# Optimization experiments

Hardware: AMD Instinct MI355X
Metric: run time of the kernel (lower is better)

Reference implementation:

```python
import jax, jax.numpy as jnp
import numpy as np

N_NODES, N_EDGES, NNZ = 10000, 4000, 30000
IN_CH, HEADS, OUT_CH = 128, 2, 64


def _scale2_pattern(node, edge, num_nodes, num_edges):
    """Sparsity pattern of H @ (H^T H) where H is the node x edge incidence.
    Mirrors torch.sparse.mm + coalesce + (values > 0) mask (pattern only,
    since all values are positive sums of ones)."""
    # unique incidence pattern (coalesce)
    uk = np.unique(node.astype(np.int64) * num_edges + edge.astype(np.int64))
    n_u, e_u = uk // num_edges, uk % num_edges
    # --- stage 1: pattern of H^T H = edge pairs sharing a node ---
    order = np.argsort(n_u, kind="stable")
    ns, es = n_u[order], e_u[order]
    _, starts, cnts = np.unique(ns, return_index=True, return_counts=True)
    cpe = np.repeat(cnts, cnts)          # group size per sorted entry
    gpe = np.repeat(starts, cnts)        # group start per sorted entry
    tot = int(cpe.sum())
    within = np.arange(tot) - np.repeat(np.cumsum(cpe) - cpe, cpe)
    pe = np.repeat(es, cpe)
    pep = es[np.repeat(gpe, cpe) + within]
    pk = np.unique(pe * num_edges + pep)
    pe, pep = pk // num_edges, pk % num_edges
    # --- stage 2: pattern of H @ (H^T H) ---
    po = np.argsort(pe, kind="stable")
    pe_s, pep_s = pe[po], pep[po]
    cnt_e = np.bincount(pe_s, minlength=num_edges)
    ptr = np.concatenate([np.zeros(1, np.int64), np.cumsum(cnt_e)])
    c2 = cnt_e[e_u]
    tot2 = int(c2.sum())
    within2 = np.arange(tot2) - np.repeat(np.cumsum(c2) - c2, c2)
    v2 = np.repeat(n_u, c2)
    ep2 = pep_s[ptr[e_u].repeat(c2) + within2]
    k2 = np.unique(v2 * num_edges + ep2)
    return k2 // num_edges, k2 % num_edges


def setup_inputs() -> dict:
    rng = np.random.default_rng(0)
    node1 = rng.integers(0, N_NODES, NNZ).astype(np.int64)
    edge1 = rng.integers(0, N_EDGES, NNZ).astype(np.int64)
    node2, edge2 = _scale2_pattern(node1, edge1, N_NODES, N_EDGES)

    key = jax.random.key(0)
    k = jax.random.split(key, 4)
    HO = HEADS * OUT_CH
    xav1 = (2.0 / (IN_CH + HO)) ** 0.5
    xavo = (2.0 / (HO + OUT_CH)) ** 0.5
    return {
        "x": jax.random.normal(k[0], (N_NODES, IN_CH), jnp.float32),
        "hyperedge_index1": jnp.asarray(np.stack([node1, edge1]), jnp.int32),
        "hyperedge_index2": jnp.asarray(np.stack([node2, edge2]), jnp.int32),
        "W1": jax.random.normal(k[1], (HO, IN_CH), jnp.float32) * xav1,
        "b1": jnp.zeros((HO,), jnp.float32),
        "W2": jax.random.normal(k[2], (HO, IN_CH), jnp.float32) * xav1,
        "b2": jnp.zeros((HO,), jnp.float32),
        "Wout": jax.random.normal(k[3], (OUT_CH, HO), jnp.float32) * xavo,
        "bout": jnp.zeros((OUT_CH,), jnp.float32),
        "num_edges": N_EDGES,
    }


def _hconv(x, W, b, node_idx, edge_idx, num_edges):
    num_nodes = x.shape[0]
    xt = x @ W.T + b                                  # [N, H*O]
    g = xt[node_idx]                                  # [nnz, H*O] gather
    esum = jax.ops.segment_sum(g, edge_idx, num_segments=num_edges)
    cnt = jax.ops.segment_sum(jnp.ones(edge_idx.shape, xt.dtype), edge_idx,
                              num_segments=num_edges)
    emean = esum / jnp.maximum(cnt, 1.0)[:, None]     # scatter_mean (0 if empty)
    return jax.ops.segment_sum(emean[edge_idx], node_idx,
                               num_segments=num_nodes)  # scatter_add


def reference(x, hyperedge_index1, hyperedge_index2, W1, b1, W2, b2, Wout, bout,
              num_edges):
    o1 = _hconv(x, W1, b1, hyperedge_index1[0], hyperedge_index1[1], num_edges)
    o2 = _hconv(x, W2, b2, hyperedge_index2[0], hyperedge_index2[1], num_edges)
    o = 0.5 * (o1 + o2)                               # mean over 2 scales
    return o @ Wout.T + bout                          # output_proj
```

## Files before the change

kernel.cpp:

```cpp
#include <hip/hip_runtime.h>
#include <hip/hip_bf16.h>

#define N_NODES 10000
#define N_EDGES 4000
#define IN_CH   128
#define CHUNK   16384

#define G_GEMM  625
#define G_NPTR  40

__device__ __forceinline__ float bf2f(unsigned short u) {
    union { unsigned int i; float f; } v;
    v.i = ((unsigned int)u) << 16;
    return v.f;
}
__device__ __forceinline__ unsigned short f2bfu(float f) {
    union { __hip_bfloat16 h; unsigned short u; } v;
    v.h = __float2bfloat16(f);
    return v.u;
}

__device__ __forceinline__ void load8(const void* base, size_t eoff, int isf32,
                                      float o[8]) {
    if (isf32) {
        const float4* q = (const float4*)((const float*)base + eoff);
        float4 a = q[0], b = q[1];
        o[0]=a.x; o[1]=a.y; o[2]=a.z; o[3]=a.w;
        o[4]=b.x; o[5]=b.y; o[6]=b.z; o[7]=b.w;
    } else {
        uint4 v = *(const uint4*)((const unsigned short*)base + eoff);
        const unsigned short* pv = (const unsigned short*)&v;
#pragma unroll
        for (int q = 0; q < 8; q++) o[q] = bf2f(pv[q]);
    }
}

__device__ __forceinline__ float loadS(const void* base, int i, int isf32) {
    return isf32 ? ((const float*)base)[i] : bf2f(((const unsigned short*)base)[i]);
}

__device__ __forceinline__ int probe_isf32(const unsigned int* __restrict__ x) {
    const int lane = threadIdx.x & 63;
    unsigned int w0 = x[lane * 2], w1 = x[lane * 2 + 1];
    int h = 0, z = 0;
    {
        unsigned int lo = w0 & 0xFFFFu;
        if (lo == 0u) z++; else if (((lo >> 7) & 0xFF) >= 0x90u) h++;
        lo = w1 & 0xFFFFu;
        if (lo == 0u) z++; else if (((lo >> 7) & 0xFF) >= 0x90u) h++;
    }
    unsigned long long bh = __ballot(h > 0);
    unsigned long long bz = __ballot(z == 2);
    return (__popcll(bh) > 8 || __popcll(bz) > 50) ? 1 : 0;
}

__device__ __forceinline__ void add4(float acc[4], uint2 u) {
    acc[0] += bf2f((unsigned short)(u.x & 0xFFFFu));
    acc[1] += bf2f((unsigned short)(u.x >> 16));
    acc[2] += bf2f((unsigned short)(u.y & 0xFFFFu));
    acc[3] += bf2f((unsigned short)(u.y >> 16));
}

__device__ __forceinline__ void block_scan(const int* __restrict__ cnt, int nb,
                                           int* __restrict__ out,
                                           int* __restrict__ part)
{
    const int t = threadIdx.x;
    const int K = (nb + 255) >> 8;
    const int base = t * K;
    int s = 0;
    for (int q = 0; q < K; q++) { int i = base + q; s += (i < nb) ? cnt[i] : 0; }
    part[t] = s;
    __syncthreads();
    for (int d = 1; d < 256; d <<= 1) {
        int v = (t >= d) ? part[t - d] : 0;
        __syncthreads();
        part[t] += v;
        __syncthreads();
    }
    int run = part[t] - s;
    for (int q = 0; q < K; q++) {
        int i = base + q;
        if (i < nb) { out[i] = run; run += cnt[i]; }
    }
    if (t == 255) out[nb] = part[255];
    __syncthreads();
}

__global__ __launch_bounds__(256) void weff_zero(
    const void* __restrict__ Wout,
    const void* __restrict__ W1, const void* __restrict__ b1,
    const void* __restrict__ W2, const void* __restrict__ b2,
    float* __restrict__ weff1, float* __restrict__ beff1,
    float* __restrict__ weff2, float* __restrict__ beff2,
    int* __restrict__ cntz, int* __restrict__ fillz,
    const unsigned int* __restrict__ xprobe)
{
    const int b = blockIdx.x;
    if (b == 4) {
        for (int t = threadIdx.x; t < 18000; t += 256) cntz[t] = 0;
        for (int t = threadIdx.x; t < 14000; t += 256) fillz[t] = 0;
        return;
    }
    __shared__ float wsh[64][IN_CH];
    const int isf32 = probe_isf32(xprobe);

    if (b == 5) {
        float* bsh = &wsh[0][0];
        const int t = threadIdx.x;
        {
            const int s = t >> 7, h = t & 127;
            bsh[t] = loadS(s ? b2 : b1, h, isf32);
        }
        __syncthreads();
        if (t < 128) {
            const int s = t >> 6, o = t & 63;
            float a = 0.f;
#pragma unroll 4
            for (int r = 0; r < 16; r++) {
                float v[8];
                load8(Wout, (size_t)o * 128 + r * 8, isf32, v);
#pragma unroll
                for (int q = 0; q < 8; q++) a += v[q] * bsh[s * 128 + r * 8 + q];
            }
            (s ? beff2 : beff1)[o] = 0.5f * a;
        }
        return;
    }

    const int s  = b >> 1;
    const int oh = b & 1;
    const void* Ws = s ? W2 : W1;
    float* outW = s ? weff2 : weff1;
    const int o  = oh * 32 + (threadIdx.x >> 3);
    const int i0 = (threadIdx.x & 7) * 16;
    float acc[16];
#pragma unroll
    for (int k = 0; k < 16; k++) acc[k] = 0.f;

    for (int pass = 0; pass < 2; pass++) {
        if (pass) __syncthreads();
        for (int r = 0; r < 4; r++) {
            int idx = r * 2048 + threadIdx.x * 8;
            float v[8];
            load8(Ws, (size_t)pass * 8192 + idx, isf32, v);
            float* d = &wsh[0][0] + idx;
#pragma unroll
            for (int q = 0; q < 8; q++) d[q] = v[q];
        }
        float wrow[64];
#pragma unroll
        for (int r = 0; r < 8; r++) {
            float v[8];
            load8(Wout, (size_t)o * 128 + pass * 64 + r * 8, isf32, v);
#pragma unroll
            for (int q = 0; q < 8; q++) wrow[r * 8 + q] = v[q];
        }
        __syncthreads();
#pragma unroll 4
        for (int h = 0; h < 64; h++) {
            const float wo = wrow[h];
            const float* wr = &wsh[h][i0];
#pragma unroll
            for (int k = 0; k < 16; k++) acc[k] += wo * wr[k];
        }
    }
#pragma unroll
    for (int k = 0; k < 16; k++)
        outW[o * 128 + i0 + k] = 0.5f * acc[k];
}

__global__ __launch_bounds__(256) void prep(
    const void* __restrict__ x,
    const float* __restrict__ weff1, const float* __restrict__ beff1,
    const float* __restrict__ weff2, const float* __restrict__ beff2,
    unsigned short* __restrict__ xtP1b, unsigned short* __restrict__ xtP2b,
    const int* __restrict__ idx1, int nnz1,
    const int* __restrict__ idx2, int nnz2,
    int* __restrict__ nptr,
    int* __restrict__ bh, int* __restrict__ cnt2,
    int* __restrict__ cnt1e, int* __restrict__ cnt1n, int nblk)
{
    __shared__ __align__(16) char smem[40000];
    int b = blockIdx.x;

    if (b < nblk) {
        int* h = (int*)smem;
        for (int t = threadIdx.x; t < N_EDGES; t += 256) h[t] = 0;
        __syncthreads();
        const int lo = b * CHUNK;
        const int hi = min(nnz2, lo + CHUNK);
        for (int i = lo + threadIdx.x; i < hi; i += 256)
            atomicAdd(&h[idx2[nnz2 + i]], 1);
        __syncthreads();
        int* dst = bh + (size_t)b * N_EDGES;
        for (int t = threadIdx.x; t < N_EDGES; t += 256) {
            int v = h[t];
            dst[t] = v;
            if (v) atomicAdd(&cnt2[t], v);
        }
        return;
    }
    b -= nblk;

    if (b < 8) {
        const int isEdge = b < 4;
        const int bid = isEdge ? b : (b - 4);
        const int nb = isEdge ? N_EDGES : N_NODES;
        const int* src = isEdge ? (idx1 + nnz1) : idx1;
        int* dst = isEdge ? cnt1e : cnt1n;
        int* h = (int*)smem;
        for (int t = threadIdx.x; t < nb; t += 256) h[t] = 0;
        __syncthreads();
        for (int i = bid * 256 + threadIdx.x; i < nnz1; i += 4 * 256)
            atomicAdd(&h[src[i]], 1);
        __syncthreads();
        for (int t = threadIdx.x; t < nb; t += 256) {
            int v = h[t];
            if (v) atomicAdd(&dst[t], v);
        }
        return;
    }
    b -= 8;

    if (b < G_GEMM) {
        const int isf32 = probe_isf32((const unsigned int*)x);
        float (*xs)[IN_CH] = (float (*)[IN_CH])smem;
        const int n0 = b * 16;
        {
            float v[8];
            load8(x, (size_t)n0 * IN_CH + (size_t)threadIdx.x * 8, isf32, v);
            float* dst = &xs[0][0] + threadIdx.x * 8;
#pragma unroll
            for (int q = 0; q < 8; q++) dst[q] = v[q];
        }
        __syncthreads();

        const int g   = threadIdx.x >> 7;
        const int sel = (threadIdx.x >> 6) & 1;
        const int j   = threadIdx.x & 63;
        const float* WE = sel ? weff2 : weff1;
        const float* BE = sel ? beff2 : beff1;
        unsigned short* xtP = sel ? xtP2b : xtP1b;

        float acc[8];
#pragma unroll
        for (int m = 0; m < 8; m++) acc[m] = 0.f;

        const float4* Wr = (const float4*)(WE + (size_t)j * 128);
        for (int kk = 0; kk < 16; kk++) {
            float4 a = Wr[kk * 2], c = Wr[kk * 2 + 1];
            float w[8] = {a.x, a.y, a.z, a.w, c.x, c.y, c.z, c.w};
#pragma unroll
            for (int m = 0; m < 8; m++) {
                const float* xr = &xs[g * 8 + m][kk * 8];
                acc[m] += xr[0]*w[0] + xr[1]*w[1] + xr[2]*w[2] + xr[3]*w[3]
                        + xr[4]*w[4] + xr[5]*w[5] + xr[6]*w[6] + xr[7]*w[7];
            }
        }
        const float bias = BE[j];
#pragma unroll
        for (int m = 0; m < 8; m++)
            xtP[(size_t)(n0 + g * 8 + m) * 64 + j] = f2bfu(acc[m] + bias);
        return;
    }
    b -= G_GEMM;

    {
        int n = b * 256 + threadIdx.x;
        if (n > N_NODES) return;
        int lo = 0, hi = nnz2;
        while (lo < hi) { int mid = (lo + hi) >> 1; if (idx2[mid] < n) lo = mid + 1; else hi = mid; }
        nptr[n] = lo;
    }
}

__global__ __launch_bounds__(256) void sb_fb2(
    const int* __restrict__ cnt2, int* __restrict__ ptr2g,
    int* __restrict__ bh, int nblk,
    const int* __restrict__ idx1, int nnz1,
    const int* __restrict__ cnt1e, int* __restrict__ ptr1eg,
    int* __restrict__ fill1e, unsigned short* __restrict__ nodelist1,
    const int* __restrict__ cnt1n, int* __restrict__ ptr1ng,
    int* __restrict__ fill1n, unsigned short* __restrict__ edgelist1)
{
    __shared__ int sscan[14002];
    __shared__ int part[256];
    int b = blockIdx.x;
    const int t = threadIdx.x;

    if (b < 16) {
        block_scan(cnt2, N_EDGES, sscan, part);
        if (b == 0)
            for (int i = t; i <= N_EDGES; i += 256) ptr2g[i] = sscan[i];
        int e = b * 256 + t;
        if (e < N_EDGES) {
            int run = sscan[e];
            int k = 0;
            for (; k + 8 <= nblk; k += 8) {
                int v[8];
#pragma unroll
                for (int q = 0; q < 8; q++)
                    v[q] = bh[(size_t)(k + q) * N_EDGES + e];
#pragma unroll
                for (int q = 0; q < 8; q++) {
                    bh[(size_t)(k + q) * N_EDGES + e] = run;
                    run += v[q];
                }
            }
            for (; k < nblk; k++) {
                int i = k * N_EDGES + e;
                int tmp = bh[i];
                bh[i] = run;
                run += tmp;
            }
        }
        return;
    }
    b -= 16;
    int* p1e = sscan;
    int* p1n = sscan + 4001;
    block_scan(cnt1e, N_EDGES, p1e, part);
    block_scan(cnt1n, N_NODES, p1n, part);
    if (b == 0) {
        for (int i = t; i <= N_EDGES; i += 256) ptr1eg[i] = p1e[i];
        for (int i = t; i <= N_NODES; i += 256) ptr1ng[i] = p1n[i];
    }
    int i = b * 256 + t;
    if (i >= nnz1) return;
    int n = idx1[i];
    int e = idx1[nnz1 + i];
    int se = atomicAdd(&fill1e[e], 1);
    nodelist1[p1e[e] + se] = (unsigned short)n;
    int sn = atomicAdd(&fill1n[n], 1);
    edgelist1[p1n[n] + sn] = (unsigned short)e;
}

__global__ __launch_bounds__(1024) void place_entries(
    const int* __restrict__ idx, int nnz, const int* __restrict__ bh,
    unsigned short* __restrict__ nodelist)
{
    __shared__ int lh[N_EDGES];
    for (int t = threadIdx.x; t < N_EDGES; t += 1024) lh[t] = 0;
    __syncthreads();
    const int b = blockIdx.x;
    const int lo = b * CHUNK;
    const int hi = min(nnz, lo + CHUNK);
    const int* bhb = bh + (size_t)b * N_EDGES;
    for (int i = lo + threadIdx.x; i < hi; i += 1024) {
        int n = idx[i];
        int e = idx[nnz + i];
        int s = atomicAdd(&lh[e], 1);
        nodelist[bhb[e] + s] = (unsigned short)n;
    }
}

__global__ __launch_bounds__(256) void edge_gather(
    const unsigned short* __restrict__ nodelist2, const int* __restrict__ ptr2,
    const unsigned int* __restrict__ xtP2u, unsigned int* __restrict__ emean2b,
    const unsigned short* __restrict__ nodelist1, const int* __restrict__ ptr1e,
    const unsigned int* __restrict__ xtP1u, unsigned int* __restrict__ emean1b)
{
    int b = blockIdx.x;
    if (b < 1000) {
        const int lane = threadIdx.x & 63;
        const int sub  = lane >> 4;
        const int ch4  = lane & 15;
        const int e = b * 4 + (threadIdx.x >> 6);
        const int lo = ptr2[e], hi = ptr2[e + 1];
        const uint2* src2 = (const uint2*)xtP2u;
        float acc[4] = {0.f, 0.f, 0.f, 0.f};
        int i = lo;
        for (; i + 32 <= hi; i += 32) {
            int n[8]; uint2 u[8];
#pragma unroll
            for (int q = 0; q < 8; q++) n[q] = nodelist2[i + 4 * q + sub];
#pragma unroll
            for (int q = 0; q < 8; q++) u[q] = src2[(size_t)n[q] * 16 + ch4];
#pragma unroll
            for (int q = 0; q < 8; q++) add4(acc, u[q]);
        }
        for (; i < hi; i += 4) {
            if (i + sub < hi) {
                int n0 = nodelist2[i + sub];
                add4(acc, src2[(size_t)n0 * 16 + ch4]);
            }
        }
#pragma unroll
        for (int q = 0; q < 4; q++) {
            acc[q] += __shfl_xor(acc[q], 16);
            acc[q] += __shfl_xor(acc[q], 32);
        }
        if (sub == 0) {
            const float inv = 1.f / fmaxf((float)(hi - lo), 1.f);
            uint2 o;
            o.x = ((unsigned int)f2bfu(acc[1] * inv) << 16) | f2bfu(acc[0] * inv);
            o.y = ((unsigned int)f2bfu(acc[3] * inv) << 16) | f2bfu(acc[2] * inv);
            ((uint2*)emean2b)[(size_t)e * 16 + ch4] = o;
        }
        return;
    }
    b -= 1000;
    {
        const int lane = threadIdx.x & 31;
        const int e = b * 8 + (threadIdx.x >> 5);
        const int lo = ptr1e[e], hi = ptr1e[e + 1];
        float accx = 0.f, accy = 0.f;
        for (int base = lo; base < hi; base += 32) {
            const int m = min(32, hi - base);
            int vl = (base + lane < hi) ? (int)nodelist1[base + lane] : 0;
            int t = 0;
            for (; t + 7 < m; t += 8) {
                int nn[8]; unsigned int uu[8];
#pragma unroll
                for (int q = 0; q < 8; q++) nn[q] = __shfl(vl, t + q, 32);
#pragma unroll
                for (int q = 0; q < 8; q++) uu[q] = xtP1u[nn[q] * 32 + lane];
#pragma unroll
                for (int q = 0; q < 8; q++) {
                    accx += bf2f((unsigned short)(uu[q] & 0xFFFFu));
                    accy += bf2f((unsigned short)(uu[q] >> 16));
                }
            }
            for (; t < m; t++) {
                int n = __shfl(vl, t, 32);
                unsigned int u = xtP1u[n * 32 + lane];
                accx += bf2f((unsigned short)(u & 0xFFFFu));
                accy += bf2f((unsigned short)(u >> 16));
            }
        }
        const float inv = 1.f / fmaxf((float)(hi - lo), 1.f);
        emean1b[e * 32 + lane] =
            ((unsigned int)f2bfu(accy * inv) << 16) | f2bfu(accx * inv);
    }
}

__global__ __launch_bounds__(256) void node_final(
    const int* __restrict__ vals2, const int* __restrict__ nptr,
    const unsigned int* __restrict__ emean2b,
    const unsigned short* __restrict__ edgelist1, const int* __restrict__ ptr1n,
    const unsigned int* __restrict__ emean1b,
    const void* __restrict__ bout, void* __restrict__ out,
    const unsigned int* __restrict__ xprobe)
{
    const int isf32 = probe_isf32(xprobe);
    const int lane = threadIdx.x & 63;
    const int sub  = lane >> 4;
    const int ch4  = lane & 15;
    const int n = blockIdx.x * 4 + (threadIdx.x >> 6);
    float acc[4] = {0.f, 0.f, 0.f, 0.f};

    {
        const int lo = nptr[n], hi = nptr[n + 1];
        const uint2* src = (const uint2*)emean2b;
        int i = lo;
        for (; i + 32 <= hi; i += 32) {
            int e[8]; uint2 u[8];
#pragma unroll
            for (int q = 0; q < 8; q++) e[q] = vals2[i + 4 * q + sub];
#pragma unroll
            for (int q = 0; q < 8; q++) u[q] = src[(size_t)e[q] * 16 + ch4];
#pragma unroll
            for (int q = 0; q < 8; q++) add4(acc, u[q]);
        }
        for (; i < hi; i += 4) {
            if (i + sub < hi)
                add4(acc, src[(size_t)vals2[i + sub] * 16 + ch4]);
        }
    }
    {
        const int lo = ptr1n[n], hi = ptr1n[n + 1];
        const uint2* src = (const uint2*)emean1b;
        int i = lo;
        for (; i + 32 <= hi; i += 32) {
            int e[8]; uint2 u[8];
#pragma unroll
            for (int q = 0; q < 8; q++) e[q] = edgelist1[i + 4 * q + sub];
#pragma unroll
            for (int q = 0; q < 8; q++) u[q] = src[(size_t)e[q] * 16 + ch4];
#pragma unroll
            for (int q = 0; q < 8; q++) add4(acc, u[q]);
        }
        for (; i < hi; i += 4) {
            if (i + sub < hi)
                add4(acc, src[(size_t)edgelist1[i + sub] * 16 + ch4]);
        }
    }
#pragma unroll
    for (int q = 0; q < 4; q++) {
        acc[q] += __shfl_xor(acc[q], 16);
        acc[q] += __shfl_xor(acc[q], 32);
    }
    if (sub == 0) {
        float r[4];
#pragma unroll
        for (int q = 0; q < 4; q++)
            r[q] = acc[q] + loadS(bout, ch4 * 4 + q, isf32);
        if (isf32) {
            ((float4*)out)[(size_t)n * 16 + ch4] =
                make_float4(r[0], r[1], r[2], r[3]);
        } else {
            uint2 o;
            o.x = ((unsigned int)f2bfu(r[1]) << 16) | f2bfu(r[0]);
            o.y = ((unsigned int)f2bfu(r[3]) << 16) | f2bfu(r[2]);
            ((uint2*)out)[(size_t)n * 16 + ch4] = o;
        }
    }
}

extern "C" void kernel_launch(void* const* d_in, const int* in_sizes, int n_in,
                              void* d_out, int out_size, void* d_ws, size_t ws_size,
                              hipStream_t stream)
{
    const void* x  = d_in[0];
    const int* idx1 = (const int*)d_in[1];
    const int* idx2 = (const int*)d_in[2];
    const void* W1 = d_in[3];
    const void* b1 = d_in[4];
    const void* W2 = d_in[5];
    const void* b2 = d_in[6];
    const void* Wo = d_in[7];
    const void* bo = d_in[8];

    const int nnz1 = in_sizes[1] / 2;
    const int nnz2 = in_sizes[2] / 2;
    const int nblk = (nnz2 + CHUNK - 1) / CHUNK;

    float* ws = (float*)d_ws;
    unsigned short* xtP1b = (unsigned short*)ws;
    unsigned int*   xtP1u = (unsigned int*)xtP1b;
    unsigned short* xtP2b = (unsigned short*)(ws + 320000);
    unsigned int*   xtP2u = (unsigned int*)xtP2b;
    int*   fill1e = (int*)(ws + 1280000);
    int*   fill1n = (int*)(ws + 1284000);
    int* cnt2  = (int*)(ws + 1550000);
    int* cnt1e = (int*)(ws + 1554000);
    int* cnt1n = (int*)(ws + 1558000);
    int* ptr2  = (int*)(ws + 1568000);
    int* ptr1e = (int*)(ws + 1572004);
    int* ptr1n = (int*)(ws + 1576008);
    int* nptr  = (int*)(ws + 1586012);
    float* weff1 = ws + 1596016;
    float* weff2 = ws + 1604208;
    float* beff1 = ws + 1612400;
    float* beff2 = ws + 1612464;
    unsigned int* emean2b = (unsigned int*)(ws + 1612528);
    unsigned int* emean1b = (unsigned int*)(ws + 1740528);
    unsigned short* nodelist2 = (unsigned short*)(ws + 1868528);
    const size_t nl2u = ((size_t)nnz2 + 1) / 2;
    unsigned short* nodelist1 = (unsigned short*)(ws + 1868528 + nl2u);
    const size_t nl1u = ((size_t)nnz1 + 1) / 2;
    unsigned short* edgelist1 = (unsigned short*)(ws + 1868528 + nl2u + nl1u);
    const size_t bh_off = (1868528 + nl2u + 2 * nl1u + 7) & ~(size_t)7;
    int* bh = (int*)(ws + bh_off);

    weff_zero<<<6, 256, 0, stream>>>(Wo, W1, b1, W2, b2,
                                     weff1, beff1, weff2, beff2,
                                     cnt2, fill1e, (const unsigned int*)x);

    prep<<<nblk + 8 + G_GEMM + G_NPTR, 256, 0, stream>>>(
        x, weff1, beff1, weff2, beff2, xtP1b, xtP2b,
        idx1, nnz1, idx2, nnz2,
        nptr, bh, cnt2, cnt1e, cnt1n, nblk);

    sb_fb2<<<16 + (nnz1 + 255) / 256, 256, 0, stream>>>(
        cnt2, ptr2, bh, nblk,
        idx1, nnz1,
        cnt1e, ptr1e, fill1e, nodelist1,
        cnt1n, ptr1n, fill1n, edgelist1);

    place_entries<<<nblk, 1024, 0, stream>>>(idx2, nnz2, bh, nodelist2);

    edge_gather<<<1000 + N_EDGES / 8, 256, 0, stream>>>(
        nodelist2, ptr2, xtP2u, emean2b,
        nodelist1, ptr1e, xtP1u, emean1b);

    node_final<<<N_NODES / 4, 256, 0, stream>>>(
        idx2 + nnz2, nptr, emean2b, edgelist1, ptr1n, emean1b,
        bo, d_out, (const unsigned int*)x);
}
```

Before: 192.6 us.

## Fuse block-histogram offset scan into scale-2 placement kernel, dropping a launch

Merges the per-edge cross-block prefix pass and the place_entries kernel into one 1024-thread kernel. Each placement block now computes its own per-edge offsets by summing the histograms of earlier blocks, then scatters its chunk's entries. The scale-1 fill blocks move to the same 1024-thread kernel. This removes one kernel launch and its dependency boundary. In exchange, the work to compute offsets grows with the number of blocks (block b reads b histograms), and the scale-1 path now uses larger blocks with a longer scan.

```diff
diff --git a/kernel.cpp b/kernel.cpp
--- a/kernel.cpp
+++ b/kernel.cpp
@@ -61,18 +61,18 @@
     acc[3] += bf2f((unsigned short)(u.y >> 16));
 }
 
-__device__ __forceinline__ void block_scan(const int* __restrict__ cnt, int nb,
-                                           int* __restrict__ out,
-                                           int* __restrict__ part)
+__device__ __forceinline__ void block_scan1024(const int* __restrict__ cnt,
+                                               int nb, int* __restrict__ out,
+                                               int* __restrict__ part)
 {
     const int t = threadIdx.x;
-    const int K = (nb + 255) >> 8;
+    const int K = (nb + 1023) >> 10;
     const int base = t * K;
     int s = 0;
     for (int q = 0; q < K; q++) { int i = base + q; s += (i < nb) ? cnt[i] : 0; }
     part[t] = s;
     __syncthreads();
-    for (int d = 1; d < 256; d <<= 1) {
+    for (int d = 1; d < 1024; d <<= 1) {
         int v = (t >= d) ? part[t - d] : 0;
         __syncthreads();
         part[t] += v;
@@ -83,7 +83,7 @@
         int i = base + q;
         if (i < nb) { out[i] = run; run += cnt[i]; }
     }
-    if (t == 255) out[nb] = part[255];
+    if (t == 1023) out[nb] = part[1023];
     __syncthreads();
 }
 
@@ -275,9 +275,11 @@
     }
 }
 
-__global__ __launch_bounds__(256) void sb_fb2(
+__global__ __launch_bounds__(1024) void sort_fill(
     const int* __restrict__ cnt2, int* __restrict__ ptr2g,
-    int* __restrict__ bh, int nblk,
+    const int* __restrict__ bh, int nblk,
+    const int* __restrict__ idx2, int nnz2,
+    unsigned short* __restrict__ nodelist2,
     const int* __restrict__ idx1, int nnz1,
     const int* __restrict__ cnt1e, int* __restrict__ ptr1eg,
     int* __restrict__ fill1e, unsigned short* __restrict__ nodelist1,
@@ -285,48 +287,42 @@
     int* __restrict__ fill1n, unsigned short* __restrict__ edgelist1)
 {
     __shared__ int sscan[14002];
-    __shared__ int part[256];
+    __shared__ int part[1024];
     int b = blockIdx.x;
     const int t = threadIdx.x;
 
-    if (b < 16) {
-        block_scan(cnt2, N_EDGES, sscan, part);
+    if (b < nblk) {
+        block_scan1024(cnt2, N_EDGES, sscan, part);
         if (b == 0)
-            for (int i = t; i <= N_EDGES; i += 256) ptr2g[i] = sscan[i];
-        int e = b * 256 + t;
-        if (e < N_EDGES) {
-            int run = sscan[e];
-            int k = 0;
-            for (; k + 8 <= nblk; k += 8) {
-                int v[8];
-#pragma unroll
-                for (int q = 0; q < 8; q++)
-                    v[q] = bh[(size_t)(k + q) * N_EDGES + e];
-#pragma unroll
-                for (int q = 0; q < 8; q++) {
-                    bh[(size_t)(k + q) * N_EDGES + e] = run;
-                    run += v[q];
-                }
-            }
-            for (; k < nblk; k++) {
-                int i = k * N_EDGES + e;
-                int tmp = bh[i];
-                bh[i] = run;
-                run += tmp;
-            }
-        }
-        return;
-    }
-    b -= 16;
+            for (int i = t; i <= N_EDGES; i += 1024) ptr2g[i] = sscan[i];
+        int* lh = sscan + 4001;
+        for (int e = t; e < N_EDGES; e += 1024) {
+            int acc = sscan[e];
+            for (int k = 0; k < b; k++) acc += bh[(size_t)k * N_EDGES + e];
+            sscan[e] = acc;
+            lh[e] = 0;
+        }
+        __syncthreads();
+        const int lo = b * CHUNK;
+        const int hi = min(nnz2, lo + CHUNK);
+        for (int i = lo + t; i < hi; i += 1024) {
+            int n = idx2[i];
+            int e = idx2[nnz2 + i];
+            int s = atomicAdd(&lh[e], 1);
+            nodelist2[sscan[e] + s] = (unsigned short)n;
+        }
+        return;
+    }
+    b -= nblk;
     int* p1e = sscan;
     int* p1n = sscan + 4001;
-    block_scan(cnt1e, N_EDGES, p1e, part);
-    block_scan(cnt1n, N_NODES, p1n, part);
+    block_scan1024(cnt1e, N_EDGES, p1e, part);
+    block_scan1024(cnt1n, N_NODES, p1n, part);
     if (b == 0) {
-        for (int i = t; i <= N_EDGES; i += 256) ptr1eg[i] = p1e[i];
-        for (int i = t; i <= N_NODES; i += 256) ptr1ng[i] = p1n[i];
-    }
-    int i = b * 256 + t;
+        for (int i = t; i <= N_EDGES; i += 1024) ptr1eg[i] = p1e[i];
+        for (int i = t; i <= N_NODES; i += 1024) ptr1ng[i] = p1n[i];
+    }
+    int i = b * 1024 + t;
     if (i >= nnz1) return;
     int n = idx1[i];
     int e = idx1[nnz1 + i];
@@ -334,25 +330,6 @@
     nodelist1[p1e[e] + se] = (unsigned short)n;
     int sn = atomicAdd(&fill1n[n], 1);
     edgelist1[p1n[n] + sn] = (unsigned short)e;
-}
-
-__global__ __launch_bounds__(1024) void place_entries(
-    const int* __restrict__ idx, int nnz, const int* __restrict__ bh,
-    unsigned short* __restrict__ nodelist)
-{
-    __shared__ int lh[N_EDGES];
-    for (int t = threadIdx.x; t < N_EDGES; t += 1024) lh[t] = 0;
-    __syncthreads();
-    const int b = blockIdx.x;
-    const int lo = b * CHUNK;
-    const int hi = min(nnz, lo + CHUNK);
-    const int* bhb = bh + (size_t)b * N_EDGES;
-    for (int i = lo + threadIdx.x; i < hi; i += 1024) {
-        int n = idx[i];
-        int e = idx[nnz + i];
-        int s = atomicAdd(&lh[e], 1);
-        nodelist[bhb[e] + s] = (unsigned short)n;
-    }
 }
 
 __global__ __launch_bounds__(256) void edge_gather(
@@ -525,6 +502,7 @@
     const int nnz1 = in_sizes[1] / 2;
     const int nnz2 = in_sizes[2] / 2;
     const int nblk = (nnz2 + CHUNK - 1) / CHUNK;
+    const int F1p = (nnz1 + 1023) / 1024;
 
     float* ws = (float*)d_ws;
     unsigned short* xtP1b = (unsigned short*)ws;
@@ -563,14 +541,13 @@
         idx1, nnz1, idx2, nnz2,
         nptr, bh, cnt2, cnt1e, cnt1n, nblk);
 
-    sb_fb2<<<16 + (nnz1 + 255) / 256, 256, 0, stream>>>(
+    sort_fill<<<nblk + F1p, 1024, 0, stream>>>(
         cnt2, ptr2, bh, nblk,
+        idx2, nnz2, nodelist2,
         idx1, nnz1,
         cnt1e, ptr1e, fill1e, nodelist1,
         cnt1n, ptr1n, fill1n, edgelist1);
 
-    place_entries<<<nblk, 1024, 0, stream>>>(idx2, nnz2, bh, nodelist2);
-
     edge_gather<<<1000 + N_EDGES / 8, 256, 0, stream>>>(
         nodelist2, ptr2, xtP2u, emean2b,
         nodelist1, ptr1e, xtP1u, emean1b);
```

After: 187.5 us. 1.03x faster.
